# Optimization experiments

Hardware: AMD Instinct MI355X
Metric: run time of the kernel (lower is better)

The kernel has to match this reference:

```python
import jax, jax.numpy as jnp
import numpy as np

EMBED_DIM = 128

def setup_inputs() -> dict:
    key = jax.random.key(0)
    k_x, k_wf, k_bf, k_wo, k_bo = jax.random.split(key, 5)
    C = EMBED_DIM
    x = jax.random.normal(k_x, (4, 4096, C), dtype=jnp.float32)
    # Linear(C, 3C): weight applied as x @ W_fc + b_fc with W_fc [C, 3C]
    W_fc = jax.random.normal(k_wf, (C, 3 * C), dtype=jnp.float32) * (1.0 / np.sqrt(C))
    b_fc = jax.random.normal(k_bf, (3 * C,), dtype=jnp.float32) * 0.01
    W_out = jax.random.normal(k_wo, (C, C), dtype=jnp.float32) * (1.0 / np.sqrt(C))
    b_out = jax.random.normal(k_bo, (C,), dtype=jnp.float32) * 0.01
    scale = jnp.ones((1,), dtype=jnp.float32)
    return {"x": x, "W_fc": W_fc, "b_fc": b_fc, "W_out": W_out, "b_out": b_out, "scale": scale}

def reference(x, W_fc, b_fc, W_out, b_out, scale):
    C = x.shape[-1]
    qkv = x @ W_fc + b_fc                      # [B, N, 3C]
    q, k, v = jnp.split(qkv, 3, axis=-1)       # each [B, N, C]
    # scores: [B, N, N], scaled by 1/sqrt(C) then by learnable 1/scale
    attn = jnp.einsum('bnc,bmc->bnm', q, k) / jnp.sqrt(jnp.float32(C))
    attn = jax.nn.softmax(attn / scale[0], axis=-1)
    out = jnp.einsum('bnm,bmc->bnc', attn, v)   # [B, N, C]
    return out @ W_out + b_out
```

## Files before the change

kernel.cpp:

```cpp
#include <hip/hip_runtime.h>
#include <math.h>


typedef __attribute__((ext_vector_type(8))) short bf16x8;
typedef __attribute__((ext_vector_type(4))) short bf16x4;
typedef __attribute__((ext_vector_type(4))) float f32x4;

#define M2EXP 17.3124f

static __device__ __forceinline__ short f2bf(float f) {
    union { float f; unsigned int u; } c; c.f = f;
    unsigned int u = c.u;
    unsigned int r = (u + 0x7FFFu + ((u >> 16) & 1u)) >> 16;
    return (short)(r & 0xFFFFu);
}
static __device__ __forceinline__ float bf2f(short v) {
    union { unsigned int u; float f; } c;
    c.u = ((unsigned int)(unsigned short)v) << 16;
    return c.f;
}

__global__ void transpose_w(const float* __restrict__ Wfc, const float* __restrict__ Wout,
                            short* __restrict__ WfcT, short* __restrict__ WoT) {
    int id = blockIdx.x * 256 + threadIdx.x;
    if (id < 384 * 128) {
        int n = id >> 7, k = id & 127;
        WfcT[id] = f2bf(Wfc[k * 384 + n]);
    } else {
        int id2 = id - 384 * 128;
        if (id2 < 128 * 128) {
            int n = id2 >> 7, k = id2 & 127;
            WoT[id2] = f2bf(Wout[k * 128 + n]);
        }
    }
}

__global__ __launch_bounds__(256) void qkv_kernel(
    const float* __restrict__ x, const short* __restrict__ WfcT,
    const float* __restrict__ bfc, const float* __restrict__ scale,
    short* __restrict__ Qs, short* __restrict__ Kb, short* __restrict__ VT) {
    __shared__ short Xs[16][136];
    const int t = threadIdx.x;
    const int rb = blockIdx.x;
    const int cb = blockIdx.y;
    const int lane = t & 63, w = t >> 6;
    const int m16 = lane & 15, quad = lane >> 4;
    {
        int row = t >> 4, col = (t & 15) * 8;
        const float* src = &x[(rb * 16 + row) * 128 + col];
        float4 f0 = *(const float4*)&src[0];
        float4 f1 = *(const float4*)&src[4];
        bf16x8 v;
        v[0] = f2bf(f0.x); v[1] = f2bf(f0.y); v[2] = f2bf(f0.z); v[3] = f2bf(f0.w);
        v[4] = f2bf(f1.x); v[5] = f2bf(f1.y); v[6] = f2bf(f1.z); v[7] = f2bf(f1.w);
        *(bf16x8*)&Xs[row][col] = v;
    }
    __syncthreads();

    f32x4 acc[2];
    for (int i = 0; i < 2; ++i)
        for (int j = 0; j < 4; ++j) acc[i][j] = 0.0f;

    const short* wbase = WfcT + (cb * 128) * 128;
    for (int kc = 0; kc < 4; ++kc) {
        bf16x8 a = *(const bf16x8*)&Xs[m16][kc * 32 + quad * 8];
        for (int c2 = 0; c2 < 2; ++c2) {
            int ct = w * 2 + c2;
            bf16x8 b = *(const bf16x8*)&wbase[(ct * 16 + m16) * 128 + kc * 32 + quad * 8];
            acc[c2] = __builtin_amdgcn_mfma_f32_16x16x32_bf16(a, b, acc[c2], 0, 0, 0);
        }
    }

    float sfac = 1.44269504088896f / (sqrtf(128.0f) * scale[0]);
    const int rbase = rb * 16 + quad * 4;
    for (int c2 = 0; c2 < 2; ++c2) {
        int ct = w * 2 + c2;
        int c = cb * 128 + ct * 16 + m16;
        float bias = bfc[c];
        if (cb == 0) {
            for (int r = 0; r < 4; ++r)
                Qs[(rbase + r) * 128 + c] = f2bf((acc[c2][r] + bias) * sfac);
        } else if (cb == 1) {
            for (int r = 0; r < 4; ++r)
                Kb[(rbase + r) * 128 + (c - 128)] = f2bf(acc[c2][r] + bias);
        } else {
            int cc = c - 256;
            bf16x4 tv;
            for (int r = 0; r < 4; ++r) tv[r] = f2bf(acc[c2][r] + bias);
            int b_ = rbase >> 12;
            int nn = rbase & 4095;
            *(bf16x4*)&VT[(b_ * 128 + cc) * 4096 + nn] = tv;
        }
    }
}

__global__ __launch_bounds__(256) void flash_kernel(
    const short* __restrict__ Qs, const short* __restrict__ Kb,
    const short* __restrict__ VT, short* __restrict__ Opart,
    float* __restrict__ Lpart, int nsplit) {
    __shared__ short Kst[64 * 128];
    __shared__ short VTs[128 * 64];
    __shared__ short Ps[64 * 64];

    const int t = threadIdx.x;
    const int lane = t & 63, w = t >> 6;
    const int m16 = lane & 15, quad = lane >> 4;
    const int kvq = blockIdx.x >> 8;
    const int bqt = blockIdx.x & 255;
    const int batch = bqt & 3;
    const int qt = bqt >> 2;
    const int iters = 64 / nsplit;
    const int qlen = 4096 / nsplit;

    bf16x8 qf[4];
    {
        const short* qb = Qs + (batch * 4096 + qt * 64 + w * 16 + m16) * 128;
        for (int kc = 0; kc < 4; ++kc)
            qf[kc] = *(const bf16x8*)&qb[kc * 32 + quad * 8];
    }

    f32x4 acc_o[8];
    for (int i = 0; i < 8; ++i)
        for (int j = 0; j < 4; ++j) acc_o[i][j] = 0.0f;
    float lsum[4] = {0.f, 0.f, 0.f, 0.f};

    const short* kbase = Kb + (batch * 4096 + kvq * qlen) * 128;
    const short* vbase = VT + (batch * 128) * 4096 + kvq * qlen;

    const int krl = lane >> 4, kslot = lane & 15;
    const int vrl = lane >> 3, vslot = lane & 7;

    for (int kt = 0; kt < iters; ++kt) {
        __syncthreads();
        for (int j = 0; j < 4; ++j) {
            int krow = w * 16 + j * 4 + krl;
            int gch = kslot ^ (krow & 15);
            __builtin_amdgcn_global_load_lds(
                (const __attribute__((address_space(1))) void*)
                    &kbase[(kt * 64 + krow) * 128 + gch * 8],
                (__attribute__((address_space(3))) void*)&Kst[(w * 16 + j * 4) * 128],
                16, 0, 0);
        }
        for (int j = 0; j < 4; ++j) {
            int vrow = w * 32 + j * 8 + vrl;
            int gch = vslot ^ (vrow & 7);
            __builtin_amdgcn_global_load_lds(
                (const __attribute__((address_space(1))) void*)
                    &vbase[vrow * 4096 + kt * 64 + gch * 8],
                (__attribute__((address_space(3))) void*)&VTs[(w * 32 + j * 8) * 64],
                16, 0, 0);
        }
        __syncthreads();

        f32x4 s[4];
        for (int i = 0; i < 4; ++i)
            for (int j = 0; j < 4; ++j) s[i][j] = 0.0f;
        for (int kc = 0; kc < 4; ++kc) {
            bf16x8 a = qf[kc];
            for (int ct = 0; ct < 4; ++ct) {
                bf16x8 b = *(const bf16x8*)&Kst[(ct * 16 + m16) * 128 +
                                                (((4 * kc + quad) ^ m16) << 3)];
                s[ct] = __builtin_amdgcn_mfma_f32_16x16x32_bf16(a, b, s[ct], 0, 0, 0);
            }
        }

        for (int ct = 0; ct < 4; ++ct)
            for (int r = 0; r < 4; ++r) {
                float p = __builtin_amdgcn_exp2f(s[ct][r] - M2EXP);
                lsum[r] += p;
                int prow = w * 16 + quad * 4 + r;
                int pcol = ct * 16 + m16;
                Ps[prow * 64 + (((pcol >> 3) ^ (prow & 7)) << 3) + (pcol & 7)] = f2bf(p);
            }

        for (int kc2 = 0; kc2 < 2; ++kc2) {
            int prow = w * 16 + m16;
            bf16x8 a2 = *(const bf16x8*)&Ps[prow * 64 +
                                            (((4 * kc2 + quad) ^ (prow & 7)) << 3)];
            for (int ot = 0; ot < 8; ++ot) {
                int vr_ = ot * 16 + m16;
                bf16x8 b2 = *(const bf16x8*)&VTs[vr_ * 64 +
                                                 (((4 * kc2 + quad) ^ (vr_ & 7)) << 3)];
                acc_o[ot] = __builtin_amdgcn_mfma_f32_16x16x32_bf16(a2, b2, acc_o[ot], 0, 0, 0);
            }
        }
    }

    for (int off = 1; off < 16; off <<= 1)
        for (int r = 0; r < 4; ++r) lsum[r] += __shfl_xor(lsum[r], off, 64);

    __syncthreads();
    short* Ot = Kst;
    for (int ot = 0; ot < 8; ++ot)
        for (int r = 0; r < 4; ++r) {
            int row = w * 16 + quad * 4 + r;
            int col = ot * 16 + m16;
            Ot[row * 128 + ((((col >> 3) ^ (row & 15)) << 3)) + (col & 7)] =
                f2bf(acc_o[ot][r]);
        }
    if (m16 == 0) {
        const int rowb = batch * 4096 + qt * 64 + w * 16 + quad * 4;
        for (int r = 0; r < 4; ++r)
            Lpart[kvq * 16384 + rowb + r] = lsum[r];
    }
    __syncthreads();
    {
        short* obase = Opart + (size_t)kvq * 16384 * 128 +
                       (size_t)(batch * 4096 + qt * 64) * 128;
        int c = t & 15;
        for (int p = 0; p < 4; ++p) {
            int row = p * 16 + (t >> 4);
            uint4 v = *(const uint4*)&Ot[row * 128 + ((c ^ (row & 15)) << 3)];
            *(uint4*)&obase[row * 128 + c * 8] = v;
        }
    }
}

__global__ __launch_bounds__(256) void mergeproj_kernel(
    const short* __restrict__ Opart, const float* __restrict__ Lpart,
    const short* __restrict__ WoT, const float* __restrict__ bout,
    float* __restrict__ out, int nsplit) {
    __shared__ short Os[16][136];
    const int t = threadIdx.x;
    const int rb = blockIdx.x;
    const int lane = t & 63, w = t >> 6;
    const int m16 = lane & 15, quad = lane >> 4;
    {
        int row = rb * 16 + (t >> 4), col = (t & 15) * 8;
        float a[8] = {0, 0, 0, 0, 0, 0, 0, 0};
        float lt = 0;
        for (int q = 0; q < nsplit; ++q) {
            bf16x8 v8 = *(const bf16x8*)&Opart[((size_t)q * 16384 + row) * 128 + col];
            for (int j = 0; j < 8; ++j) a[j] += bf2f(v8[j]);
            lt += Lpart[q * 16384 + row];
        }
        float rl = 1.0f / lt;
        bf16x8 v;
        for (int j = 0; j < 8; ++j) v[j] = f2bf(a[j] * rl);
        *(bf16x8*)&Os[t >> 4][col] = v;
    }
    __syncthreads();
    f32x4 acc[2];
    for (int i = 0; i < 2; ++i)
        for (int j = 0; j < 4; ++j) acc[i][j] = 0.0f;
    for (int kc = 0; kc < 4; ++kc) {
        bf16x8 a = *(const bf16x8*)&Os[m16][kc * 32 + quad * 8];
        for (int c2 = 0; c2 < 2; ++c2) {
            int ct = w * 2 + c2;
            bf16x8 b = *(const bf16x8*)&WoT[(ct * 16 + m16) * 128 + kc * 32 + quad * 8];
            acc[c2] = __builtin_amdgcn_mfma_f32_16x16x32_bf16(a, b, acc[c2], 0, 0, 0);
        }
    }
    for (int c2 = 0; c2 < 2; ++c2) {
        int ct = w * 2 + c2;
        int c = ct * 16 + m16;
        float bias = bout[c];
        for (int r = 0; r < 4; ++r)
            out[(rb * 16 + quad * 4 + r) * 128 + c] = acc[c2][r] + bias;
    }
}

extern "C" void kernel_launch(void* const* d_in, const int* in_sizes, int n_in,
                              void* d_out, int out_size, void* d_ws, size_t ws_size,
                              hipStream_t stream) {
    const float* x     = (const float*)d_in[0];
    const float* Wfc   = (const float*)d_in[1];
    const float* bfc   = (const float*)d_in[2];
    const float* Wout  = (const float*)d_in[3];
    const float* bout  = (const float*)d_in[4];
    const float* scale = (const float*)d_in[5];
    float* out = (float*)d_out;

    char* ws = (char*)d_ws;
    short* WfcT = (short*)(ws);
    short* WoT  = (short*)(ws + 98304);
    short* Qs   = (short*)(ws + 131072);
    short* Kb   = (short*)(ws + 131072 + 4194304);
    short* VT   = (short*)(ws + 131072 + 2 * 4194304);
    const size_t base = 131072 + (size_t)3 * 4194304;
    short* Opart = (short*)(ws + base);
    const size_t opart1 = (size_t)16384 * 128 * 2;
    const size_t lpart1 = (size_t)16384 * 4;
    int nsplit;
    if (ws_size >= base + 4 * opart1 + 4 * lpart1) nsplit = 4;
    else if (ws_size >= base + 2 * opart1 + 2 * lpart1) nsplit = 2;
    else nsplit = 1;
    float* Lpart = (float*)(ws + base + (size_t)nsplit * opart1);

    hipLaunchKernelGGL(transpose_w, dim3(256), dim3(256), 0, stream, Wfc, Wout, WfcT, WoT);
    hipLaunchKernelGGL(qkv_kernel, dim3(1024, 3), dim3(256), 0, stream, x, WfcT, bfc, scale, Qs, Kb, VT);
    hipLaunchKernelGGL(flash_kernel, dim3(256 * nsplit), dim3(256), 0, stream,
                       Qs, Kb, VT, Opart, Lpart, nsplit);
    hipLaunchKernelGGL(mergeproj_kernel, dim3(1024), dim3(256), 0, stream,
                       Opart, Lpart, WoT, bout, out, nsplit);
}
```

Baseline: 156.9 us.

## Switch flash kernel to 32x32 MFMA tiles with 128-row query blocks and more KV splits

The attention kernel moves from 16x16x32 to 32x32x16 bf16 MFMA. Each wave now owns 32 query rows, so one block covers 128 queries instead of 64. With half as many blocks per split, the KV split count rises to 8 when the workspace allows, and launch bounds cap occupancy at 1. The aim is to reuse more data per LDS read and raise MFMA efficiency, at the cost of higher register pressure and more partial results to merge. The nsplit=1 fallback is removed, which would give wrong results if the workspace is too small.

```diff
diff --git a/kernel.cpp b/kernel.cpp
--- a/kernel.cpp
+++ b/kernel.cpp
@@ -5,6 +5,7 @@
 typedef __attribute__((ext_vector_type(8))) short bf16x8;
 typedef __attribute__((ext_vector_type(4))) short bf16x4;
 typedef __attribute__((ext_vector_type(4))) float f32x4;
+typedef __attribute__((ext_vector_type(16))) float f32x16;
 
 #define M2EXP 17.3124f
 
@@ -94,35 +95,37 @@
     }
 }
 
-__global__ __launch_bounds__(256) void flash_kernel(
+__global__ __launch_bounds__(256, 1) void flash_kernel(
     const short* __restrict__ Qs, const short* __restrict__ Kb,
     const short* __restrict__ VT, short* __restrict__ Opart,
     float* __restrict__ Lpart, int nsplit) {
-    __shared__ short Kst[64 * 128];
-    __shared__ short VTs[128 * 64];
-    __shared__ short Ps[64 * 64];
+    __shared__ short smem[24576];
+    short* Kst = smem;
+    short* VTs = smem + 8192;
+    short* Ps  = smem + 16384;
 
     const int t = threadIdx.x;
     const int lane = t & 63, w = t >> 6;
-    const int m16 = lane & 15, quad = lane >> 4;
-    const int kvq = blockIdx.x >> 8;
-    const int bqt = blockIdx.x & 255;
+    const int l31 = lane & 31, half = lane >> 5;
+    const int kvq = blockIdx.x >> 7;
+    const int bqt = blockIdx.x & 127;
     const int batch = bqt & 3;
     const int qt = bqt >> 2;
-    const int iters = 64 / nsplit;
     const int qlen = 4096 / nsplit;
-
-    bf16x8 qf[4];
+    const int iters = qlen / 64;
+
+    bf16x8 qf[8];
     {
-        const short* qb = Qs + (batch * 4096 + qt * 64 + w * 16 + m16) * 128;
-        for (int kc = 0; kc < 4; ++kc)
-            qf[kc] = *(const bf16x8*)&qb[kc * 32 + quad * 8];
-    }
-
-    f32x4 acc_o[8];
-    for (int i = 0; i < 8; ++i)
-        for (int j = 0; j < 4; ++j) acc_o[i][j] = 0.0f;
-    float lsum[4] = {0.f, 0.f, 0.f, 0.f};
+        const short* qb = Qs + (batch * 4096 + qt * 128 + w * 32 + l31) * 128;
+        for (int kc = 0; kc < 8; ++kc)
+            qf[kc] = *(const bf16x8*)&qb[kc * 16 + half * 8];
+    }
+
+    f32x16 acc_o[4];
+    for (int i = 0; i < 4; ++i)
+        for (int j = 0; j < 16; ++j) acc_o[i][j] = 0.0f;
+    float lsum[16];
+    for (int r = 0; r < 16; ++r) lsum[r] = 0.0f;
 
     const short* kbase = Kb + (batch * 4096 + kvq * qlen) * 128;
     const short* vbase = VT + (batch * 128) * 4096 + kvq * qlen;
@@ -152,64 +155,67 @@
         }
         __syncthreads();
 
-        f32x4 s[4];
-        for (int i = 0; i < 4; ++i)
-            for (int j = 0; j < 4; ++j) s[i][j] = 0.0f;
-        for (int kc = 0; kc < 4; ++kc) {
+        f32x16 s[2];
+        for (int i = 0; i < 2; ++i)
+            for (int j = 0; j < 16; ++j) s[i][j] = 0.0f;
+        for (int kc = 0; kc < 8; ++kc) {
             bf16x8 a = qf[kc];
-            for (int ct = 0; ct < 4; ++ct) {
-                bf16x8 b = *(const bf16x8*)&Kst[(ct * 16 + m16) * 128 +
-                                                (((4 * kc + quad) ^ m16) << 3)];
-                s[ct] = __builtin_amdgcn_mfma_f32_16x16x32_bf16(a, b, s[ct], 0, 0, 0);
+            for (int ct = 0; ct < 2; ++ct) {
+                int row = ct * 32 + l31;
+                bf16x8 b = *(const bf16x8*)&Kst[row * 128 +
+                                                (((kc * 2 + half) ^ (row & 15)) << 3)];
+                s[ct] = __builtin_amdgcn_mfma_f32_32x32x16_bf16(a, b, s[ct], 0, 0, 0);
             }
         }
 
-        for (int ct = 0; ct < 4; ++ct)
-            for (int r = 0; r < 4; ++r) {
+        for (int ct = 0; ct < 2; ++ct)
+            for (int r = 0; r < 16; ++r) {
                 float p = __builtin_amdgcn_exp2f(s[ct][r] - M2EXP);
                 lsum[r] += p;
-                int prow = w * 16 + quad * 4 + r;
-                int pcol = ct * 16 + m16;
+                int prow = w * 32 + (r & 3) + 8 * (r >> 2) + 4 * half;
+                int pcol = ct * 32 + l31;
                 Ps[prow * 64 + (((pcol >> 3) ^ (prow & 7)) << 3) + (pcol & 7)] = f2bf(p);
             }
 
-        for (int kc2 = 0; kc2 < 2; ++kc2) {
-            int prow = w * 16 + m16;
+        for (int kc2 = 0; kc2 < 4; ++kc2) {
+            int prow = w * 32 + l31;
             bf16x8 a2 = *(const bf16x8*)&Ps[prow * 64 +
-                                            (((4 * kc2 + quad) ^ (prow & 7)) << 3)];
-            for (int ot = 0; ot < 8; ++ot) {
-                int vr_ = ot * 16 + m16;
+                                            (((kc2 * 2 + half) ^ (prow & 7)) << 3)];
+            for (int ot = 0; ot < 4; ++ot) {
+                int vr_ = ot * 32 + l31;
                 bf16x8 b2 = *(const bf16x8*)&VTs[vr_ * 64 +
-                                                 (((4 * kc2 + quad) ^ (vr_ & 7)) << 3)];
-                acc_o[ot] = __builtin_amdgcn_mfma_f32_16x16x32_bf16(a2, b2, acc_o[ot], 0, 0, 0);
+                                                 (((kc2 * 2 + half) ^ (vr_ & 7)) << 3)];
+                acc_o[ot] = __builtin_amdgcn_mfma_f32_32x32x16_bf16(a2, b2, acc_o[ot], 0, 0, 0);
             }
         }
     }
 
-    for (int off = 1; off < 16; off <<= 1)
-        for (int r = 0; r < 4; ++r) lsum[r] += __shfl_xor(lsum[r], off, 64);
+    for (int off = 1; off < 32; off <<= 1)
+        for (int r = 0; r < 16; ++r) lsum[r] += __shfl_xor(lsum[r], off, 64);
+
+    if (l31 == 0) {
+        for (int r = 0; r < 16; ++r) {
+            int row_l = w * 32 + (r & 3) + 8 * (r >> 2) + 4 * half;
+            Lpart[kvq * 16384 + batch * 4096 + qt * 128 + row_l] = lsum[r];
+        }
+    }
 
     __syncthreads();
-    short* Ot = Kst;
-    for (int ot = 0; ot < 8; ++ot)
-        for (int r = 0; r < 4; ++r) {
-            int row = w * 16 + quad * 4 + r;
-            int col = ot * 16 + m16;
-            Ot[row * 128 + ((((col >> 3) ^ (row & 15)) << 3)) + (col & 7)] =
+    short* Ot = smem;
+    for (int ot = 0; ot < 4; ++ot)
+        for (int r = 0; r < 16; ++r) {
+            int row = w * 32 + (r & 3) + 8 * (r >> 2) + 4 * half;
+            int col = ot * 32 + l31;
+            Ot[row * 128 + (((col >> 3) ^ (row & 15)) << 3) + (col & 7)] =
                 f2bf(acc_o[ot][r]);
         }
-    if (m16 == 0) {
-        const int rowb = batch * 4096 + qt * 64 + w * 16 + quad * 4;
-        for (int r = 0; r < 4; ++r)
-            Lpart[kvq * 16384 + rowb + r] = lsum[r];
-    }
     __syncthreads();
     {
         short* obase = Opart + (size_t)kvq * 16384 * 128 +
-                       (size_t)(batch * 4096 + qt * 64) * 128;
+                       (size_t)(batch * 4096 + qt * 128) * 128;
         int c = t & 15;
-        for (int p = 0; p < 4; ++p) {
-            int row = p * 16 + (t >> 4);
+        for (int i = 0; i < 8; ++i) {
+            int row = i * 16 + (t >> 4);
             uint4 v = *(const uint4*)&Ot[row * 128 + ((c ^ (row & 15)) << 3)];
             *(uint4*)&obase[row * 128 + c * 8] = v;
         }
@@ -282,14 +288,14 @@
     const size_t opart1 = (size_t)16384 * 128 * 2;
     const size_t lpart1 = (size_t)16384 * 4;
     int nsplit;
-    if (ws_size >= base + 4 * opart1 + 4 * lpart1) nsplit = 4;
-    else if (ws_size >= base + 2 * opart1 + 2 * lpart1) nsplit = 2;
-    else nsplit = 1;
+    if (ws_size >= base + 8 * (opart1 + lpart1)) nsplit = 8;
+    else if (ws_size >= base + 4 * (opart1 + lpart1)) nsplit = 4;
+    else nsplit = 2;
     float* Lpart = (float*)(ws + base + (size_t)nsplit * opart1);
 
     hipLaunchKernelGGL(transpose_w, dim3(256), dim3(256), 0, stream, Wfc, Wout, WfcT, WoT);
     hipLaunchKernelGGL(qkv_kernel, dim3(1024, 3), dim3(256), 0, stream, x, WfcT, bfc, scale, Qs, Kb, VT);
-    hipLaunchKernelGGL(flash_kernel, dim3(256 * nsplit), dim3(256), 0, stream,
+    hipLaunchKernelGGL(flash_kernel, dim3(128 * nsplit), dim3(256), 0, stream,
                        Qs, Kb, VT, Opart, Lpart, nsplit);
     hipLaunchKernelGGL(mergeproj_kernel, dim3(1024), dim3(256), 0, stream,
                        Opart, Lpart, WoT, bout, out, nsplit);
```

Measured after the change: 174.6 us. 1.11x slower.
